# Performance work log

Measured on AMD Instinct MI355X. Metric: run time of the kernel, lower is better.

Reference implementation:

```python
import jax, jax.numpy as jnp
import numpy as np

N_NODES = 100000
N_EDGES = 600000
D_IN = 128
D_HID = 128
NB_LAYERS = 3
EPS = 1e-5  # torch LayerNorm default


def setup_inputs() -> dict:
    key = jax.random.key(0)
    ks = jax.random.split(key, 12)
    x = jax.random.normal(ks[0], (N_NODES, D_IN), dtype=jnp.float32)
    edge_index = jax.random.randint(ks[1], (2, N_EDGES), 0, N_NODES, dtype=jnp.int32)
    # MLP sizes: [2*D_IN, D_HID, D_HID, D_HID, 1]
    sizes = [2 * D_IN] + [D_HID] * NB_LAYERS + [1]
    inp = {"x": x, "edge_index": edge_index}
    for i in range(len(sizes) - 1):
        scale = 1.0 / np.sqrt(sizes[i]).astype(np.float32)
        inp[f"W{i}"] = jax.random.normal(ks[2 + i], (sizes[i], sizes[i + 1]), dtype=jnp.float32) * scale
        inp[f"b{i}"] = jnp.zeros((sizes[i + 1],), dtype=jnp.float32)
    for i in range(NB_LAYERS):
        inp[f"g{i}"] = jnp.ones((D_HID,), dtype=jnp.float32)      # LayerNorm gamma
        inp[f"beta{i}"] = jnp.zeros((D_HID,), dtype=jnp.float32)  # LayerNorm beta
    return inp


def _layernorm(h, g, b):
    mu = jnp.mean(h, axis=-1, keepdims=True)
    var = jnp.var(h, axis=-1, keepdims=True)
    return (h - mu) * jax.lax.rsqrt(var + EPS) * g + b


def reference(x, edge_index, W0, b0, W1, b1, W2, b2, W3, b3, g0, beta0, g1, beta1, g2, beta2):
    start, end = edge_index[0], edge_index[1]
    # gather node pairs and concat -> [E, 2*D_IN]
    h = jnp.concatenate([x[start], x[end]], axis=1)
    for W, b, g, be in ((W0, b0, g0, beta0), (W1, b1, g1, beta1), (W2, b2, g2, beta2)):
        h = jnp.tanh(_layernorm(h @ W + b, g, be))
    return (h @ W3 + b3).squeeze(-1)  # [E]
```

## Files before the change

### kernel.cpp

```cpp
#include <hip/hip_runtime.h>
#include <hip/hip_bf16.h>


typedef float f32x2 __attribute__((ext_vector_type(2)));
typedef float f32x4 __attribute__((ext_vector_type(4)));
typedef __bf16 bf16x8 __attribute__((ext_vector_type(8)));
typedef unsigned int u32x4 __attribute__((ext_vector_type(4)));

#define MFMA16(a, b, c) __builtin_amdgcn_mfma_f32_16x16x32_bf16((a), (b), (c), 0, 0, 0)

static __device__ __forceinline__ unsigned short bf16bits(float f) {
  __bf16 h = (__bf16)f;
  return __builtin_bit_cast(unsigned short, h);
}

static __device__ __forceinline__ unsigned pack2(float a, float b) {
  return (unsigned)bf16bits(a) | ((unsigned)bf16bits(b) << 16);
}

static __device__ __forceinline__ void gload_lds16(const void* g, void* l) {
  __builtin_amdgcn_global_load_lds(
      (const __attribute__((address_space(1))) void*)g,
      (__attribute__((address_space(3))) void*)l, 16, 0, 0);
}

static __device__ __forceinline__ int permk(int k) {
  const int j = k & 7, g = (k >> 3) & 3;
  return (k & ~31) | ((j >> 2) << 4) | (g << 2) | (j & 3);
}

__global__ void prep_x(const float* __restrict__ x,
                       unsigned short* __restrict__ xb, int n8) {
  int gid = blockIdx.x * blockDim.x + threadIdx.x;
  const int stride = gridDim.x * blockDim.x;
  for (int i = gid; i < n8; i += stride) {
    const float4 a = ((const float4*)x)[i * 2];
    const float4 b = ((const float4*)x)[i * 2 + 1];
    u32x4 o;
    o[0] = pack2(a.x, a.y); o[1] = pack2(a.z, a.w);
    o[2] = pack2(b.x, b.y); o[3] = pack2(b.z, b.w);
    ((u32x4*)xb)[i] = o;
  }
}

__global__ void prep_w(const float* __restrict__ W0, const float* __restrict__ W1,
                       const float* __restrict__ W2,
                       const float* __restrict__ B0, const float* __restrict__ G0,
                       const float* __restrict__ Q0,
                       const float* __restrict__ B1, const float* __restrict__ G1,
                       const float* __restrict__ Q1,
                       const float* __restrict__ B2, const float* __restrict__ G2,
                       const float* __restrict__ Q2,
                       const float* __restrict__ W3,
                       unsigned short* __restrict__ wt, float* __restrict__ pp) {
  const int t = blockIdx.x;
  const int tid = threadIdx.x;
  if (t == 8) {
    for (int i = tid; i < 1280; i += 256) {
      const int a = i >> 7, o = i & 127;
      float v;
      switch (a) {
        case 0: v = B0[o]; break;  case 1: v = G0[o]; break;
        case 2: v = Q0[o]; break;  case 3: v = B1[o]; break;
        case 4: v = G1[o]; break;  case 5: v = Q1[o]; break;
        case 6: v = B2[o]; break;  case 7: v = G2[o]; break;
        case 8: v = Q2[o]; break;  default: v = W3[o]; break;
      }
      pp[i] = v;
    }
    return;
  }
  const float* src; int kbase; int perm;
  if (t < 4)      { src = W0; kbase = t * 64;      perm = 0; }
  else if (t < 6) { src = W1; kbase = (t - 4) * 64; perm = 1; }
  else            { src = W2; kbase = (t - 6) * 64; perm = 1; }
  char* base = (char*)wt + t * 16384;
  const int col = tid & 127;
  const int kb  = (tid >> 7) << 1;
  #pragma unroll
  for (int i = 0; i < 16; ++i) {
    const int kl = kb + (i << 2);
    const int k0 = kbase + kl;
    const int c0 = perm ? permk(k0) : k0;
    const float wa = src[c0 * 128 + col];
    const float wb = src[(c0 + 1) * 128 + col];
    const unsigned pk = pack2(wa, wb);
    const int off = ((col * 64 + kl) * 2) ^ ((col & 7) << 4);
    *(unsigned*)(base + off) = pk;
  }
}

#define P_B0 0
#define P_G0 128
#define P_Q0 256
#define P_B1 384
#define P_G1 512
#define P_Q1 640
#define P_B2 768
#define P_G2 896
#define P_Q2 1024
#define P_W3 1152

template <int XB>
__global__ __launch_bounds__(256, 4) void edge_mlp(
    const float* __restrict__ x, const int* __restrict__ ei,
    const float* __restrict__ B3,
    const unsigned short* __restrict__ wt, const float* __restrict__ pp,
    const unsigned short* __restrict__ xb,
    float* __restrict__ out, int nE)
{
  __shared__ __align__(16) char lds[32768 + 5120];
  float* plds = (float*)(lds + 32768);
  const int tid  = threadIdx.x;
  const int lane = tid & 63;
  const int wv   = tid >> 6;
  const int e    = lane & 15;
  const int g    = lane >> 4;

  const int wbase = blockIdx.x * 64 + wv * 16;
  const int e0 = wbase + e;
  const int ec0 = e0 < nE ? e0 : nE - 1;
  const int ns0 = ei[ec0], ne0 = ei[nE + ec0];

  auto stageW = [&](int t, int buf) {
    #pragma unroll
    for (int c = 0; c < 4; ++c) {
      const int o = wv * 4096 + c * 1024;
      gload_lds16((const char*)wt + t * 16384 + o + lane * 16,
                  lds + buf * 16384 + o);
    }
  };

  auto loadW = [&](int buf, int m, int kl) -> bf16x8 {
    const int col = m * 16 + e;
    const int off = ((col * 64 + kl) * 2) ^ ((col & 7) << 4);
    return *(const bf16x8*)(lds + buf * 16384 + off);
  };

  auto loadX = [&](int node, int ko) -> bf16x8 {
    if (XB) {
      return *(const bf16x8*)(xb + (size_t)node * 128 + ko);
    } else {
      const float* src = x + (size_t)node * 128 + ko;
      const float4 ua = *(const float4*)(src);
      const float4 ub = *(const float4*)(src + 4);
      bf16x8 a;
      a[0] = (__bf16)ua.x; a[1] = (__bf16)ua.y; a[2] = (__bf16)ua.z; a[3] = (__bf16)ua.w;
      a[4] = (__bf16)ub.x; a[5] = (__bf16)ub.y; a[6] = (__bf16)ub.z; a[7] = (__bf16)ub.w;
      return a;
    }
  };

  f32x4 acc[8];

  auto initAcc = [&](int pb) {
    #pragma unroll
    for (int m = 0; m < 8; ++m)
      acc[m] = *(const f32x4*)(plds + pb + m * 16 + g * 4);
  };

  auto l0step = [&](int u0, int buf) {
    #pragma unroll
    for (int du = 0; du < 2; ++du) {
      const int u = u0 + du;
      const int ko = (u & 3) * 32 + g * 8;
      const bf16x8 xf = loadX(u < 4 ? ns0 : ne0, ko);
      const int kl = du * 32 + g * 8;
      #pragma unroll
      for (int m = 0; m < 8; ++m) {
        const bf16x8 wf = loadW(buf, m, kl);
        acc[m] = MFMA16(wf, xf, acc[m]);
      }
    }
  };

  unsigned p0[8], p1[8];

  auto epi = [&](int pg, int pq) {
    f32x2 s1 = {0.f, 0.f}, s2 = {0.f, 0.f};
    #pragma unroll
    for (int m = 0; m < 8; ++m) {
      const f32x2 lo = {acc[m][0], acc[m][1]};
      const f32x2 hi = {acc[m][2], acc[m][3]};
      s1 += lo; s1 += hi;
      s2 = __builtin_elementwise_fma(lo, lo, s2);
      s2 = __builtin_elementwise_fma(hi, hi, s2);
    }
    float sh1 = s1[0] + s1[1], sh2 = s2[0] + s2[1];
    sh1 += __shfl_xor(sh1, 16); sh2 += __shfl_xor(sh2, 16);
    sh1 += __shfl_xor(sh1, 32); sh2 += __shfl_xor(sh2, 32);
    const float mu  = sh1 * 0.0078125f;
    const float inv = __builtin_amdgcn_rsqf(sh2 * 0.0078125f - mu * mu + 1e-5f);
    const f32x2 mu2 = {mu, mu}, inv2 = {inv, inv};
    const f32x2 one2 = {1.f, 1.f}, negtwo2 = {-2.f, -2.f};
    #pragma unroll
    for (int m = 0; m < 8; ++m) {
      #pragma unroll
      for (int h = 0; h < 2; ++h) {
        const f32x2 a  = {acc[m][2 * h], acc[m][2 * h + 1]};
        const f32x2 gq = *(const f32x2*)(plds + pg + m * 16 + g * 4 + 2 * h);
        const f32x2 qq = *(const f32x2*)(plds + pq + m * 16 + g * 4 + 2 * h);
        const f32x2 k1 = inv2 * gq;
        f32x2 z = __builtin_elementwise_fma(a - mu2, k1, qq);
        z += z;
        const f32x2 ex  = {__expf(z[0]), __expf(z[1])};
        const f32x2 den = ex + one2;
        const f32x2 rc  = {__builtin_amdgcn_rcpf(den[0]),
                           __builtin_amdgcn_rcpf(den[1])};
        const f32x2 th  = __builtin_elementwise_fma(negtwo2, rc, one2);
        if (h == 0) p0[m] = pack2(th[0], th[1]);
        else        p1[m] = pack2(th[0], th[1]);
      }
    }
  };

  auto lstep = [&](int u0, int buf) {
    #pragma unroll
    for (int du = 0; du < 2; ++du) {
      const int u = u0 + du;
      const int kl = du * 32 + g * 8;
      u32x4 w;
      w[0] = p0[2 * u];     w[1] = p1[2 * u];
      w[2] = p0[2 * u + 1]; w[3] = p1[2 * u + 1];
      const bf16x8 bfv = __builtin_bit_cast(bf16x8, w);
      #pragma unroll
      for (int m = 0; m < 8; ++m) {
        const bf16x8 wf = loadW(buf, m, kl);
        acc[m] = MFMA16(wf, bfv, acc[m]);
      }
    }
  };

  stageW(0, 0);
  for (int i = tid; i < 1280; i += 256) plds[i] = pp[i];
  __syncthreads();

  initAcc(P_B0);
  stageW(1, 1); l0step(0, 0); __syncthreads();
  stageW(2, 0); l0step(2, 1); __syncthreads();
  stageW(3, 1); l0step(4, 0); __syncthreads();
  stageW(4, 0); l0step(6, 1); __syncthreads();
  stageW(5, 1);
  epi(P_G0, P_Q0); initAcc(P_B1); lstep(0, 0); __syncthreads();
  stageW(6, 0);
  lstep(2, 1); __syncthreads();
  stageW(7, 1);
  epi(P_G1, P_Q1); initAcc(P_B2); lstep(0, 0); __syncthreads();
  lstep(2, 1);

  const float b3v = B3[0];
  {
    f32x2 s1 = {0.f, 0.f}, s2 = {0.f, 0.f};
    #pragma unroll
    for (int m = 0; m < 8; ++m) {
      const f32x2 lo = {acc[m][0], acc[m][1]};
      const f32x2 hi = {acc[m][2], acc[m][3]};
      s1 += lo; s1 += hi;
      s2 = __builtin_elementwise_fma(lo, lo, s2);
      s2 = __builtin_elementwise_fma(hi, hi, s2);
    }
    float sh1 = s1[0] + s1[1], sh2 = s2[0] + s2[1];
    sh1 += __shfl_xor(sh1, 16); sh2 += __shfl_xor(sh2, 16);
    sh1 += __shfl_xor(sh1, 32); sh2 += __shfl_xor(sh2, 32);
    const float mu  = sh1 * 0.0078125f;
    const float inv = __builtin_amdgcn_rsqf(sh2 * 0.0078125f - mu * mu + 1e-5f);
    const f32x2 mu2 = {mu, mu}, inv2 = {inv, inv};
    const f32x2 one2 = {1.f, 1.f}, negtwo2 = {-2.f, -2.f};
    f32x2 d2 = {0.f, 0.f};
    #pragma unroll
    for (int m = 0; m < 8; ++m) {
      #pragma unroll
      for (int h = 0; h < 2; ++h) {
        const f32x2 a  = {acc[m][2 * h], acc[m][2 * h + 1]};
        const f32x2 gq = *(const f32x2*)(plds + P_G2 + m * 16 + g * 4 + 2 * h);
        const f32x2 qq = *(const f32x2*)(plds + P_Q2 + m * 16 + g * 4 + 2 * h);
        const f32x2 w3 = *(const f32x2*)(plds + P_W3 + m * 16 + g * 4 + 2 * h);
        const f32x2 k1 = inv2 * gq;
        f32x2 z = __builtin_elementwise_fma(a - mu2, k1, qq);
        z += z;
        const f32x2 ex  = {__expf(z[0]), __expf(z[1])};
        const f32x2 den = ex + one2;
        const f32x2 rc  = {__builtin_amdgcn_rcpf(den[0]),
                           __builtin_amdgcn_rcpf(den[1])};
        const f32x2 th  = __builtin_elementwise_fma(negtwo2, rc, one2);
        d2 = __builtin_elementwise_fma(th, w3, d2);
      }
    }
    float d = d2[0] + d2[1];
    d += __shfl_xor(d, 16);
    d += __shfl_xor(d, 32);
    const int eid = wbase + e;
    if (g == 0 && eid < nE) out[eid] = d + b3v;
  }
}

extern "C" void kernel_launch(void* const* d_in, const int* in_sizes, int n_in,
                              void* d_out, int out_size, void* d_ws, size_t ws_size,
                              hipStream_t stream) {
  const float* x  = (const float*)d_in[0];
  const int*   ei = (const int*)d_in[1];
  const float* W0 = (const float*)d_in[2];
  const float* B0 = (const float*)d_in[3];
  const float* W1 = (const float*)d_in[4];
  const float* B1 = (const float*)d_in[5];
  const float* W2 = (const float*)d_in[6];
  const float* B2 = (const float*)d_in[7];
  const float* W3 = (const float*)d_in[8];
  const float* B3 = (const float*)d_in[9];
  const float* G0 = (const float*)d_in[10];
  const float* Q0 = (const float*)d_in[11];
  const float* G1 = (const float*)d_in[12];
  const float* Q1 = (const float*)d_in[13];
  const float* G2 = (const float*)d_in[14];
  const float* Q2 = (const float*)d_in[15];
  float* out = (float*)d_out;

  const int nX = in_sizes[0];
  const int nE = in_sizes[1] / 2;
  const int blocks = (nE + 63) / 64;

  const size_t xb_bytes = ((size_t)nX * 2 + 255) & ~(size_t)255;
  const int use_xb = (ws_size >= xb_bytes + 131072 + 5120) ? 1 : 0;

  unsigned short* xbp = (unsigned short*)d_ws;
  unsigned short* wt  = use_xb ? (unsigned short*)((char*)d_ws + xb_bytes)
                               : (unsigned short*)d_ws;
  float* pp = (float*)((char*)wt + 131072);

  hipLaunchKernelGGL(prep_w, dim3(9), dim3(256), 0, stream,
                     W0, W1, W2, B0, G0, Q0, B1, G1, Q1, B2, G2, Q2, W3, wt, pp);
  if (use_xb) {
    hipLaunchKernelGGL(prep_x, dim3(1024), dim3(256), 0, stream, x, xbp, nX / 8);
    hipLaunchKernelGGL(edge_mlp<1>, dim3(blocks), dim3(256), 0, stream,
                       x, ei, B3, wt, pp, xbp, out, nE);
  } else {
    hipLaunchKernelGGL(edge_mlp<0>, dim3(blocks), dim3(256), 0, stream,
                       x, ei, B3, wt, pp, xbp, out, nE);
  }
}
```

Baseline: 167.5 us.

## Fold tanh scaling into LN params, read params from global, raise occupancy

LayerNorm gamma and beta are pre-scaled by 2*log2(e) in the prep kernel, so the tanh epilogue can call v_exp_f32 directly and drops the doubling and the exp scaling. The per-block LDS copy of the bias/LN/W3 parameters is removed and those values are read from global memory (cached) as 16-byte vectors, which shrinks LDS per block. Launch bounds go from 4 to 5 blocks per SM to use the freed LDS. The cost is tighter register limits, which may cause spills, and global/L1 loads in the epilogue in place of LDS reads.

```diff
diff --git a/kernel.cpp b/kernel.cpp
--- a/kernel.cpp
+++ b/kernel.cpp
@@ -8,6 +8,7 @@
 typedef unsigned int u32x4 __attribute__((ext_vector_type(4)));
 
 #define MFMA16(a, b, c) __builtin_amdgcn_mfma_f32_16x16x32_bf16((a), (b), (c), 0, 0, 0)
+#define TWO_LOG2E 2.885390081777927f
 
 static __device__ __forceinline__ unsigned short bf16bits(float f) {
   __bf16 h = (__bf16)f;
@@ -16,6 +17,12 @@
 
 static __device__ __forceinline__ unsigned pack2(float a, float b) {
   return (unsigned)bf16bits(a) | ((unsigned)bf16bits(b) << 16);
+}
+
+static __device__ __forceinline__ float exp2_fast(float z) {
+  float r;
+  asm("v_exp_f32 %0, %1" : "=v"(r) : "v"(z));
+  return r;
 }
 
 static __device__ __forceinline__ void gload_lds16(const void* g, void* l) {
@@ -60,11 +67,16 @@
       const int a = i >> 7, o = i & 127;
       float v;
       switch (a) {
-        case 0: v = B0[o]; break;  case 1: v = G0[o]; break;
-        case 2: v = Q0[o]; break;  case 3: v = B1[o]; break;
-        case 4: v = G1[o]; break;  case 5: v = Q1[o]; break;
-        case 6: v = B2[o]; break;  case 7: v = G2[o]; break;
-        case 8: v = Q2[o]; break;  default: v = W3[o]; break;
+        case 0: v = B0[o]; break;
+        case 1: v = G0[o] * TWO_LOG2E; break;
+        case 2: v = Q0[o] * TWO_LOG2E; break;
+        case 3: v = B1[o]; break;
+        case 4: v = G1[o] * TWO_LOG2E; break;
+        case 5: v = Q1[o] * TWO_LOG2E; break;
+        case 6: v = B2[o]; break;
+        case 7: v = G2[o] * TWO_LOG2E; break;
+        case 8: v = Q2[o] * TWO_LOG2E; break;
+        default: v = W3[o]; break;
       }
       pp[i] = v;
     }
@@ -102,15 +114,14 @@
 #define P_W3 1152
 
 template <int XB>
-__global__ __launch_bounds__(256, 4) void edge_mlp(
+__global__ __launch_bounds__(256, 5) void edge_mlp(
     const float* __restrict__ x, const int* __restrict__ ei,
     const float* __restrict__ B3,
     const unsigned short* __restrict__ wt, const float* __restrict__ pp,
     const unsigned short* __restrict__ xb,
     float* __restrict__ out, int nE)
 {
-  __shared__ __align__(16) char lds[32768 + 5120];
-  float* plds = (float*)(lds + 32768);
+  __shared__ __align__(16) char lds[32768];
   const int tid  = threadIdx.x;
   const int lane = tid & 63;
   const int wv   = tid >> 6;
@@ -156,7 +167,7 @@
   auto initAcc = [&](int pb) {
     #pragma unroll
     for (int m = 0; m < 8; ++m)
-      acc[m] = *(const f32x4*)(plds + pb + m * 16 + g * 4);
+      acc[m] = *(const f32x4*)(pp + pb + m * 16 + g * 4);
   };
 
   auto l0step = [&](int u0, int buf) {
@@ -195,15 +206,16 @@
     const f32x2 one2 = {1.f, 1.f}, negtwo2 = {-2.f, -2.f};
     #pragma unroll
     for (int m = 0; m < 8; ++m) {
+      const f32x4 gq4 = *(const f32x4*)(pp + pg + m * 16 + g * 4);
+      const f32x4 qq4 = *(const f32x4*)(pp + pq + m * 16 + g * 4);
       #pragma unroll
       for (int h = 0; h < 2; ++h) {
         const f32x2 a  = {acc[m][2 * h], acc[m][2 * h + 1]};
-        const f32x2 gq = *(const f32x2*)(plds + pg + m * 16 + g * 4 + 2 * h);
-        const f32x2 qq = *(const f32x2*)(plds + pq + m * 16 + g * 4 + 2 * h);
+        const f32x2 gq = {gq4[2 * h], gq4[2 * h + 1]};
+        const f32x2 qq = {qq4[2 * h], qq4[2 * h + 1]};
         const f32x2 k1 = inv2 * gq;
-        f32x2 z = __builtin_elementwise_fma(a - mu2, k1, qq);
-        z += z;
-        const f32x2 ex  = {__expf(z[0]), __expf(z[1])};
+        const f32x2 z  = __builtin_elementwise_fma(a - mu2, k1, qq);
+        const f32x2 ex  = {exp2_fast(z[0]), exp2_fast(z[1])};
         const f32x2 den = ex + one2;
         const f32x2 rc  = {__builtin_amdgcn_rcpf(den[0]),
                            __builtin_amdgcn_rcpf(den[1])};
@@ -232,7 +244,6 @@
   };
 
   stageW(0, 0);
-  for (int i = tid; i < 1280; i += 256) plds[i] = pp[i];
   __syncthreads();
 
   initAcc(P_B0);
@@ -269,16 +280,18 @@
     f32x2 d2 = {0.f, 0.f};
     #pragma unroll
     for (int m = 0; m < 8; ++m) {
+      const f32x4 gq4 = *(const f32x4*)(pp + P_G2 + m * 16 + g * 4);
+      const f32x4 qq4 = *(const f32x4*)(pp + P_Q2 + m * 16 + g * 4);
+      const f32x4 w34 = *(const f32x4*)(pp + P_W3 + m * 16 + g * 4);
       #pragma unroll
       for (int h = 0; h < 2; ++h) {
         const f32x2 a  = {acc[m][2 * h], acc[m][2 * h + 1]};
-        const f32x2 gq = *(const f32x2*)(plds + P_G2 + m * 16 + g * 4 + 2 * h);
-        const f32x2 qq = *(const f32x2*)(plds + P_Q2 + m * 16 + g * 4 + 2 * h);
-        const f32x2 w3 = *(const f32x2*)(plds + P_W3 + m * 16 + g * 4 + 2 * h);
+        const f32x2 gq = {gq4[2 * h], gq4[2 * h + 1]};
+        const f32x2 qq = {qq4[2 * h], qq4[2 * h + 1]};
+        const f32x2 w3 = {w34[2 * h], w34[2 * h + 1]};
         const f32x2 k1 = inv2 * gq;
-        f32x2 z = __builtin_elementwise_fma(a - mu2, k1, qq);
-        z += z;
-        const f32x2 ex  = {__expf(z[0]), __expf(z[1])};
+        const f32x2 z  = __builtin_elementwise_fma(a - mu2, k1, qq);
+        const f32x2 ex  = {exp2_fast(z[0]), exp2_fast(z[1])};
         const f32x2 den = ex + one2;
         const f32x2 rc  = {__builtin_amdgcn_rcpf(den[0]),
                            __builtin_amdgcn_rcpf(den[1])};
```

Result: slower. 197.7 us (+18.0%).
